# Performance work log

Hardware: AMD Instinct MI355X
Metric: run time of the kernel (lower is better)

The kernel has to match this reference:

```python
import jax, jax.numpy as jnp
import numpy as np

N_NODES = 100000
N_EDGES = 1600000
IN_DIM = 48
HID = 128
BN_EPS = 1e-5


def _batchnorm(h, gamma, beta):
    # BatchNorm1d in training mode: batch mean, biased variance
    mu = jnp.mean(h, axis=0)
    var = jnp.mean(jnp.square(h - mu), axis=0)
    return (h - mu) * jax.lax.rsqrt(var + BN_EPS) * gamma + beta


def setup_inputs() -> dict:
    key = jax.random.key(0)
    ks = jax.random.split(key, 8)
    x = jax.random.normal(ks[0], (N_NODES, IN_DIM), dtype=jnp.float32)
    edge_index = jax.random.randint(ks[1], (2, N_EDGES), 0, N_NODES, dtype=jnp.int64)
    s1 = 1.0 / np.sqrt(IN_DIM)
    s2 = 1.0 / np.sqrt(HID)
    return {
        "x": x,
        "edge_index": edge_index,
        "W1": jax.random.uniform(ks[2], (HID, IN_DIM), jnp.float32, -s1, s1),
        "b1": jnp.zeros((HID,), jnp.float32),
        "g1": jnp.ones((HID,), jnp.float32),
        "be1": jnp.zeros((HID,), jnp.float32),
        "Wl": jax.random.uniform(ks[3], (HID, HID), jnp.float32, -s2, s2),
        "bl": jnp.zeros((HID,), jnp.float32),
        "Wr": jax.random.uniform(ks[4], (HID, HID), jnp.float32, -s2, s2),
        "g2": jnp.ones((HID,), jnp.float32),
        "be2": jnp.zeros((HID,), jnp.float32),
    }


def reference(x, edge_index, W1, b1, g1, be1, Wl, bl, Wr, g2, be2):
    # input projection: Linear -> BatchNorm -> ReLU
    h = x @ W1.T + b1                               # [N, HID]
    feat = jax.nn.relu(_batchnorm(h, g1, be1))      # [N, HID]

    # SAGEConv (mean aggregation): messages flow src -> dst
    src, dst = edge_index[0], edge_index[1]
    summed = jax.ops.segment_sum(feat[src], dst, num_segments=N_NODES)  # [N, HID]
    cnt = jax.ops.segment_sum(jnp.ones((N_EDGES,), jnp.float32), dst, num_segments=N_NODES)
    agg = summed / jnp.maximum(cnt, 1.0)[:, None]
    sage = agg @ Wl.T + bl + feat @ Wr.T            # lin_l(mean) + lin_r(self)

    out_feat = _batchnorm(sage, g2, be2)
    return (feat, out_feat)
```

## Files before the change

### kernel.cpp

```cpp
#include <hip/hip_runtime.h>
#include <hip/hip_bf16.h>

#define NN 100000
#define NE 1600000
#define INDIM 48
#define HID 128
#define K2 256
#define KP 64
#define BN_EPS 1e-5f

#define NBUK 782
#define BCAP 2816
#define CHUNK 8192

#define MT ((NN + 63) / 64)
#define MT2 ((NN + 127) / 128)

typedef short s8v __attribute__((ext_vector_type(8)));
typedef float f4v __attribute__((ext_vector_type(4)));
typedef float f2v __attribute__((ext_vector_type(2)));

__device__ __forceinline__ unsigned short f2bf(float f) {
    __hip_bfloat16 b = __float2bfloat16(f);
    unsigned short u;
    __builtin_memcpy(&u, &b, 2);
    return u;
}
__device__ __forceinline__ float bflo(unsigned u) { return __uint_as_float(u << 16); }
__device__ __forceinline__ float bfhi(unsigned u) { return __uint_as_float(u & 0xffff0000u); }
__device__ __forceinline__ unsigned packbf(float lo, float hi) {
    return (unsigned)f2bf(lo) | ((unsigned)f2bf(hi) << 16);
}

__global__ __launch_bounds__(256) void k_xcast(const float* __restrict__ x,
                                               unsigned short* __restrict__ xbf,
                                               const float* __restrict__ Wl, const float* __restrict__ Wr,
                                               const float* __restrict__ W1,
                                               unsigned short* __restrict__ Wcat,
                                               unsigned short* __restrict__ W1b,
                                               int* __restrict__ bcur, float* __restrict__ stats) {
  int i = blockIdx.x * 256 + threadIdx.x;
  if (i < NN * 16) {
    int r = i >> 4, c4 = (i & 15) << 2;
    ushort4 o = {0, 0, 0, 0};
    if (c4 < INDIM) {
      float4 v = *(const float4*)(x + (size_t)r * INDIM + c4);
      o.x = f2bf(v.x);
      o.y = f2bf(v.y);
      o.z = f2bf(v.z);
      o.w = f2bf(v.w);
    }
    *(ushort4*)(xbf + (size_t)r * KP + c4) = o;
  }
  if (i < HID * K2) {
    int j = i >> 8, k = i & (K2 - 1);
    float v = (k < HID) ? Wl[j * HID + k] : Wr[j * HID + (k - HID)];
    Wcat[i] = f2bf(v);
  }
  int i2 = i - HID * K2;
  if (i2 >= 0 && i2 < HID * KP) {
    int j = i2 >> 6, k = i2 & (KP - 1);
    W1b[i2] = (k < INDIM) ? f2bf(W1[j * INDIM + k]) : (unsigned short)0;
  }
  int i3 = i2 - HID * KP;
  if (i3 >= 0 && i3 < NBUK) bcur[i3] = 0;
  int i4 = i3 - NBUK;
  if (i4 >= 0 && i4 < 4 * HID) stats[i4] = 0.f;
}

__global__ __launch_bounds__(256) void k_proj_gemm(
    const unsigned short* __restrict__ xbf, const unsigned short* __restrict__ W1b,
    const float* __restrict__ b1, unsigned short* __restrict__ Abuf,
    float* __restrict__ colSum, float* __restrict__ colSq) {
  __shared__ __align__(16) unsigned short Bsh[HID][KP + 8];
  __shared__ float redS[4][HID], redQ[4][HID];
  int tid = threadIdx.x;
  for (int i = tid; i < HID * (KP / 8); i += 256) {
    int j = i >> 3, kg = (i & 7) << 3;
    *(s8v*)&Bsh[j][kg] = *(const s8v*)(W1b + (size_t)j * KP + kg);
  }
  __syncthreads();
  int w = tid >> 6, l = tid & 63;
  int m16 = l & 15, q = l >> 4;
  float bcol[8];
#pragma unroll
  for (int nt = 0; nt < 8; ++nt) bcol[nt] = b1[nt * 16 + m16];
  float ssum[8], ssq[8];
#pragma unroll
  for (int nt = 0; nt < 8; ++nt) { ssum[nt] = 0.f; ssq[nt] = 0.f; }
  f4v zero4 = {0.f, 0.f, 0.f, 0.f};
  s8v zero8 = {0, 0, 0, 0, 0, 0, 0, 0};
  for (int tile = blockIdx.x; tile < MT; tile += gridDim.x) {
    int row = tile * 64 + w * 16 + m16;
    bool rv = row < NN;
    f4v acc[8];
#pragma unroll
    for (int nt = 0; nt < 8; ++nt) acc[nt] = zero4;
#pragma unroll
    for (int kt = 0; kt < 2; ++kt) {
      s8v a = zero8;
      if (rv) a = *(const s8v*)(xbf + (size_t)row * KP + kt * 32 + q * 8);
#pragma unroll
      for (int nt = 0; nt < 8; ++nt) {
        s8v b = *(const s8v*)(&Bsh[nt * 16 + m16][kt * 32 + q * 8]);
        acc[nt] = __builtin_amdgcn_mfma_f32_16x16x32_bf16(a, b, acc[nt], 0, 0, 0);
      }
    }
    int rbase = tile * 64 + w * 16 + q * 4;
#pragma unroll
    for (int nt = 0; nt < 8; ++nt) {
      int col = nt * 16 + m16;
#pragma unroll
      for (int r4 = 0; r4 < 4; ++r4) {
        int rr = rbase + r4;
        if (rr < NN) {
          float v = acc[nt][r4] + bcol[nt];
          Abuf[(size_t)rr * K2 + HID + col] = f2bf(v);
          ssum[nt] += v;
          ssq[nt] = fmaf(v, v, ssq[nt]);
        }
      }
    }
  }
#pragma unroll
  for (int nt = 0; nt < 8; ++nt) {
    float s = ssum[nt], qq = ssq[nt];
    s += __shfl_xor(s, 16);
    s += __shfl_xor(s, 32);
    qq += __shfl_xor(qq, 16);
    qq += __shfl_xor(qq, 32);
    if (q == 0) {
      redS[w][nt * 16 + m16] = s;
      redQ[w][nt * 16 + m16] = qq;
    }
  }
  __syncthreads();
  if (tid < HID) {
    float s = redS[0][tid] + redS[1][tid] + redS[2][tid] + redS[3][tid];
    float qq = redQ[0][tid] + redQ[1][tid] + redQ[2][tid] + redQ[3][tid];
    atomicAdd(&colSum[tid], s);
    atomicAdd(&colSq[tid], qq);
  }
}

__global__ void k_bn_final(const float* __restrict__ sum, const float* __restrict__ sq,
                           const float* __restrict__ gamma, const float* __restrict__ beta,
                           float* __restrict__ av, float* __restrict__ bv) {
  int c = threadIdx.x;
  float mu = sum[c] * (1.0f / NN);
  float var = fmaxf(sq[c] * (1.0f / NN) - mu * mu, 0.f);
  float a = gamma[c] * rsqrtf(var + BN_EPS);
  av[c] = a;
  bv[c] = beta[c] - mu * a;
}

__global__ __launch_bounds__(256) void k_apply(float* __restrict__ feat,
                                               const float* __restrict__ av,
                                               const float* __restrict__ bv,
                                               unsigned short* __restrict__ A,
                                               unsigned char* __restrict__ feat8) {
  int i = blockIdx.x * 256 + threadIdx.x;
  if (i >= NN * 16) return;
  int r = i >> 4, c8 = (i & 15) << 3;
  unsigned short* ap = A + (size_t)r * K2 + HID + c8;
  uint4 hv = *(const uint4*)ap;
  float4 a0 = *(const float4*)(av + c8);
  float4 a1 = *(const float4*)(av + c8 + 4);
  float4 b0 = *(const float4*)(bv + c8);
  float4 b1 = *(const float4*)(bv + c8 + 4);
  float f0 = fmaxf(fmaf(bflo(hv.x), a0.x, b0.x), 0.f);
  float f1 = fmaxf(fmaf(bfhi(hv.x), a0.y, b0.y), 0.f);
  float f2 = fmaxf(fmaf(bflo(hv.y), a0.z, b0.z), 0.f);
  float f3 = fmaxf(fmaf(bfhi(hv.y), a0.w, b0.w), 0.f);
  float f4 = fmaxf(fmaf(bflo(hv.z), a1.x, b1.x), 0.f);
  float f5 = fmaxf(fmaf(bfhi(hv.z), a1.y, b1.y), 0.f);
  float f6 = fmaxf(fmaf(bflo(hv.w), a1.z, b1.z), 0.f);
  float f7 = fmaxf(fmaf(bfhi(hv.w), a1.w, b1.w), 0.f);
  float4 o0 = {f0, f1, f2, f3}, o1 = {f4, f5, f6, f7};
  *(float4*)(feat + (size_t)r * HID + c8) = o0;
  *(float4*)(feat + (size_t)r * HID + c8 + 4) = o1;
  uint4 ob;
  ob.x = packbf(f0, f1);
  ob.y = packbf(f2, f3);
  ob.z = packbf(f4, f5);
  ob.w = packbf(f6, f7);
  *(uint4*)ap = ob;
  unsigned p0 = __builtin_amdgcn_cvt_pk_fp8_f32(f0, f1, 0u, false);
  p0 = __builtin_amdgcn_cvt_pk_fp8_f32(f2, f3, p0, true);
  unsigned p1 = __builtin_amdgcn_cvt_pk_fp8_f32(f4, f5, 0u, false);
  p1 = __builtin_amdgcn_cvt_pk_fp8_f32(f6, f7, p1, true);
  uint2 o8 = {p0, p1};
  *(uint2*)(feat8 + (size_t)r * HID + c8) = o8;
}

__global__ __launch_bounds__(512) void k_bucket(const int* __restrict__ ei,
                                                int* __restrict__ bcur,
                                                unsigned int* __restrict__ bbuf) {
  __shared__ int cnt[1024];
  __shared__ int sc[2][1024];
  __shared__ int ofs[1024];
  __shared__ int lcur[1024];
  __shared__ int gbase[1024];
  __shared__ unsigned int stag[CHUNK];
  __shared__ unsigned short sbkt[CHUNK];
  int tid = threadIdx.x;
  int base = blockIdx.x * CHUNK;
  int lim = min(CHUNK, NE - base);
  cnt[tid] = 0;
  cnt[tid + 512] = 0;
  __syncthreads();
#pragma unroll
  for (int i = 0; i < CHUNK / 512; ++i) {
    int e = i * 512 + tid;
    if (e < lim) {
      int d = ei[NE + base + e];
      d = min(max(d, 0), NN - 1);
      atomicAdd(&cnt[d >> 7], 1);
    }
  }
  __syncthreads();
  sc[0][tid] = cnt[tid];
  sc[0][tid + 512] = cnt[tid + 512];
  __syncthreads();
  int pp = 0;
  for (int d = 1; d < 1024; d <<= 1) {
    int a0 = sc[pp][tid];
    int a1 = sc[pp][tid + 512];
    if (tid >= d) a0 += sc[pp][tid - d];
    a1 += sc[pp][tid + 512 - d];
    sc[pp ^ 1][tid] = a0;
    sc[pp ^ 1][tid + 512] = a1;
    __syncthreads();
    pp ^= 1;
  }
  ofs[tid] = sc[pp][tid] - cnt[tid];
  ofs[tid + 512] = sc[pp][tid + 512] - cnt[tid + 512];
  lcur[tid] = ofs[tid];
  lcur[tid + 512] = ofs[tid + 512];
  if (tid < NBUK) gbase[tid] = atomicAdd(&bcur[tid], cnt[tid]);
  if (tid + 512 < NBUK) gbase[tid + 512] = atomicAdd(&bcur[tid + 512], cnt[tid + 512]);
  __syncthreads();
#pragma unroll
  for (int i = 0; i < CHUNK / 512; ++i) {
    int e = i * 512 + tid;
    if (e < lim) {
      int s = ei[base + e];
      int d = ei[NE + base + e];
      s = min(max(s, 0), NN - 1);
      d = min(max(d, 0), NN - 1);
      int b = d >> 7;
      int pos = atomicAdd(&lcur[b], 1);
      stag[pos] = (unsigned)s | ((unsigned)(d & 127) << 17);
      sbkt[pos] = (unsigned short)b;
    }
  }
  __syncthreads();
  for (int s = tid; s < lim; s += 512) {
    int b = sbkt[s];
    int off = gbase[b] + (s - ofs[b]);
    if (off < BCAP) bbuf[(size_t)b * BCAP + off] = stag[s];
  }
}

__global__ __launch_bounds__(512) void k_bucket_agg(const unsigned int* __restrict__ bbuf,
                                                    const int* __restrict__ bcnt,
                                                    const unsigned char* __restrict__ feat8,
                                                    unsigned short* __restrict__ Abuf) {
  __shared__ unsigned int lcsr[BCAP];
  __shared__ int cnt[128], ofs[128], cur[128];
  __shared__ int sc[2][128];
  int tid = threadIdx.x;
  int b = blockIdx.x;
  int m = min(bcnt[b], BCAP);
  int n0 = b << 7;
  int nb = min(128, NN - n0);
  if (tid < 128) cnt[tid] = 0;
  __syncthreads();
  const unsigned int* bp = bbuf + (size_t)b * BCAP;
  for (int s = tid; s < m; s += 512) {
    unsigned p = bp[s];
    atomicAdd(&cnt[(p >> 17) & 127], 1);
  }
  __syncthreads();
  if (tid < 128) sc[0][tid] = cnt[tid];
  __syncthreads();
  int pp = 0;
  for (int d = 1; d < 128; d <<= 1) {
    if (tid < 128) {
      int v = sc[pp][tid];
      if (tid >= d) v += sc[pp][tid - d];
      sc[pp ^ 1][tid] = v;
    }
    __syncthreads();
    pp ^= 1;
  }
  if (tid < 128) {
    int o = sc[pp][tid] - cnt[tid];
    ofs[tid] = o;
    cur[tid] = o;
  }
  __syncthreads();
  for (int s = tid; s < m; s += 512) {
    unsigned p = bp[s];
    int ld = (p >> 17) & 127;
    int pos = atomicAdd(&cur[ld], 1);
    lcsr[pos] = p & 0x1FFFF;
  }
  __syncthreads();
  int lane = tid & 31;
  int g = tid >> 5;
  int half = (lane >> 3) & 3;
  int l8 = lane & 7;
  for (int ln = g; ln < nb; ln += 16) {
    int deg = cnt[ln], beg = ofs[ln];
    float ac[16];
#pragma unroll
    for (int i = 0; i < 16; ++i) ac[i] = 0.f;
#pragma unroll 2
    for (int j = 0; j < deg; j += 4) {
      int idx = j + half;
      uint4 v = {0u, 0u, 0u, 0u};
      if (idx < deg) {
        int s = lcsr[beg + idx];
        v = *(const uint4*)(feat8 + (size_t)s * HID + l8 * 16);
      }
      f2v d;
      d = __builtin_amdgcn_cvt_pk_f32_fp8(v.x, false); ac[0] += d.x;  ac[1] += d.y;
      d = __builtin_amdgcn_cvt_pk_f32_fp8(v.x, true);  ac[2] += d.x;  ac[3] += d.y;
      d = __builtin_amdgcn_cvt_pk_f32_fp8(v.y, false); ac[4] += d.x;  ac[5] += d.y;
      d = __builtin_amdgcn_cvt_pk_f32_fp8(v.y, true);  ac[6] += d.x;  ac[7] += d.y;
      d = __builtin_amdgcn_cvt_pk_f32_fp8(v.z, false); ac[8] += d.x;  ac[9] += d.y;
      d = __builtin_amdgcn_cvt_pk_f32_fp8(v.z, true);  ac[10] += d.x; ac[11] += d.y;
      d = __builtin_amdgcn_cvt_pk_f32_fp8(v.w, false); ac[12] += d.x; ac[13] += d.y;
      d = __builtin_amdgcn_cvt_pk_f32_fp8(v.w, true);  ac[14] += d.x; ac[15] += d.y;
    }
#pragma unroll
    for (int i = 0; i < 16; ++i) {
      ac[i] += __shfl_xor(ac[i], 8);
      ac[i] += __shfl_xor(ac[i], 16);
    }
    if (half == 0) {
      float inv = 1.f / fmaxf((float)deg, 1.f);
      uint4 o0, o1;
      o0.x = packbf(ac[0] * inv, ac[1] * inv);
      o0.y = packbf(ac[2] * inv, ac[3] * inv);
      o0.z = packbf(ac[4] * inv, ac[5] * inv);
      o0.w = packbf(ac[6] * inv, ac[7] * inv);
      o1.x = packbf(ac[8] * inv, ac[9] * inv);
      o1.y = packbf(ac[10] * inv, ac[11] * inv);
      o1.z = packbf(ac[12] * inv, ac[13] * inv);
      o1.w = packbf(ac[14] * inv, ac[15] * inv);
      unsigned short* op = Abuf + (size_t)(n0 + ln) * K2 + l8 * 16;
      *(uint4*)op = o0;
      *(uint4*)(op + 8) = o1;
    }
  }
}

__global__ __launch_bounds__(512) void k_gemm(
    const unsigned short* __restrict__ A, const unsigned short* __restrict__ Wcat,
    const float* __restrict__ bl, unsigned short* __restrict__ sageb,
    float* __restrict__ colSum, float* __restrict__ colSq) {
  __shared__ __align__(16) unsigned short Bsh[HID][264];
  __shared__ float redS[8][HID], redQ[8][HID];
  int tid = threadIdx.x;
  for (int i = tid; i < HID * 32; i += 512) {
    int j = i >> 5;
    int kg = (i & 31) << 3;
    *(s8v*)&Bsh[j][kg] = *(const s8v*)(Wcat + (size_t)j * K2 + kg);
  }
  __syncthreads();
  int w = tid >> 6, l = tid & 63;
  int m16 = l & 15, q = l >> 4;
  int tile = blockIdx.x;
  int row = tile * 128 + w * 16 + m16;
  bool rv = row < NN;
  f4v zero4 = {0.f, 0.f, 0.f, 0.f};
  s8v zero8 = {0, 0, 0, 0, 0, 0, 0, 0};
  f4v acc[8];
#pragma unroll
  for (int nt = 0; nt < 8; ++nt) acc[nt] = zero4;
#pragma unroll
  for (int kt = 0; kt < 8; ++kt) {
    s8v a = zero8;
    if (rv) a = *(const s8v*)(A + (size_t)row * K2 + kt * 32 + q * 8);
#pragma unroll
    for (int nt = 0; nt < 8; ++nt) {
      s8v bfr = *(const s8v*)(&Bsh[nt * 16 + m16][kt * 32 + q * 8]);
      acc[nt] = __builtin_amdgcn_mfma_f32_16x16x32_bf16(a, bfr, acc[nt], 0, 0, 0);
    }
  }
  int rbase = tile * 128 + w * 16 + q * 4;
  float ssum[8], ssq[8];
#pragma unroll
  for (int nt = 0; nt < 8; ++nt) { ssum[nt] = 0.f; ssq[nt] = 0.f; }
#pragma unroll
  for (int nt = 0; nt < 8; ++nt) {
    int col = nt * 16 + m16;
    float bv = bl[col];
#pragma unroll
    for (int r4 = 0; r4 < 4; ++r4) {
      int rr = rbase + r4;
      if (rr < NN) {
        float v = acc[nt][r4] + bv;
        sageb[(size_t)rr * HID + col] = f2bf(v);
        ssum[nt] += v;
        ssq[nt] = fmaf(v, v, ssq[nt]);
      }
    }
  }
#pragma unroll
  for (int nt = 0; nt < 8; ++nt) {
    float s = ssum[nt], qq = ssq[nt];
    s += __shfl_xor(s, 16);
    s += __shfl_xor(s, 32);
    qq += __shfl_xor(qq, 16);
    qq += __shfl_xor(qq, 32);
    if (q == 0) {
      redS[w][nt * 16 + m16] = s;
      redQ[w][nt * 16 + m16] = qq;
    }
  }
  __syncthreads();
  if (tid < HID) {
    float s = 0.f, qq = 0.f;
#pragma unroll
    for (int ww = 0; ww < 8; ++ww) { s += redS[ww][tid]; qq += redQ[ww][tid]; }
    atomicAdd(&colSum[tid], s);
    atomicAdd(&colSq[tid], qq);
  }
}

__global__ __launch_bounds__(256) void k_bn_apply(const unsigned short* __restrict__ sageb,
                                                  float* __restrict__ out,
                                                  const float* __restrict__ av,
                                                  const float* __restrict__ bv) {
  int i = blockIdx.x * 256 + threadIdx.x;
  if (i >= NN * 16) return;
  int r = i >> 4, c8 = (i & 15) << 3;
  uint4 sv = *(const uint4*)(sageb + (size_t)r * HID + c8);
  float4 a0 = *(const float4*)(av + c8);
  float4 a1 = *(const float4*)(av + c8 + 4);
  float4 b0 = *(const float4*)(bv + c8);
  float4 b1 = *(const float4*)(bv + c8 + 4);
  float4 o0, o1;
  o0.x = fmaf(bflo(sv.x), a0.x, b0.x);
  o0.y = fmaf(bfhi(sv.x), a0.y, b0.y);
  o0.z = fmaf(bflo(sv.y), a0.z, b0.z);
  o0.w = fmaf(bfhi(sv.y), a0.w, b0.w);
  o1.x = fmaf(bflo(sv.z), a1.x, b1.x);
  o1.y = fmaf(bfhi(sv.z), a1.y, b1.y);
  o1.z = fmaf(bflo(sv.w), a1.z, b1.z);
  o1.w = fmaf(bfhi(sv.w), a1.w, b1.w);
  *(float4*)(out + (size_t)r * HID + c8) = o0;
  *(float4*)(out + (size_t)r * HID + c8 + 4) = o1;
}

extern "C" void kernel_launch(void* const* d_in, const int* in_sizes, int n_in,
                              void* d_out, int out_size, void* d_ws, size_t ws_size,
                              hipStream_t stream) {
  const float* x   = (const float*)d_in[0];
  const int*   ei  = (const int*)d_in[1];
  const float* W1  = (const float*)d_in[2];
  const float* b1  = (const float*)d_in[3];
  const float* g1  = (const float*)d_in[4];
  const float* be1 = (const float*)d_in[5];
  const float* Wl  = (const float*)d_in[6];
  const float* bl  = (const float*)d_in[7];
  const float* Wr  = (const float*)d_in[8];
  const float* g2  = (const float*)d_in[9];
  const float* be2 = (const float*)d_in[10];

  float* feat_out = (float*)d_out;
  float* out2     = (float*)d_out + (size_t)NN * HID;

  size_t off = 0;
  auto alloc = [&](size_t bytes) -> void* {
    void* p = (char*)d_ws + off;
    off += (bytes + 255) & ~(size_t)255;
    return p;
  };
  unsigned short* Abuf = (unsigned short*)alloc((size_t)NN * K2 * 2);
  unsigned char*  feat8 = (unsigned char*)alloc((size_t)NN * HID);
  unsigned short* sageb = (unsigned short*)alloc((size_t)NN * HID * 2);
  unsigned int*   bbuf = (unsigned int*)alloc((size_t)NBUK * BCAP * 4);
  int*            bcur = (int*)alloc((size_t)NBUK * 4);
  float*          stats = (float*)alloc(8 * HID * 4);
  float* colSum1 = stats;
  float* colSq1  = stats + HID;
  float* colSum2 = stats + 2 * HID;
  float* colSq2  = stats + 3 * HID;
  float* a1v     = stats + 4 * HID;
  float* b1v     = stats + 5 * HID;
  float* a2v     = stats + 6 * HID;
  float* b2v     = stats + 7 * HID;
  unsigned short* Wcat = (unsigned short*)alloc((size_t)HID * K2 * 2);
  unsigned short* W1b  = (unsigned short*)alloc((size_t)HID * KP * 2);
  unsigned short* xbf  = (unsigned short*)alloc((size_t)NN * KP * 2);

  k_xcast<<<(NN * 16 + 255) / 256, 256, 0, stream>>>(x, xbf, Wl, Wr, W1, Wcat, W1b, bcur, stats);
  k_bucket<<<(NE + CHUNK - 1) / CHUNK, 512, 0, stream>>>(ei, bcur, bbuf);
  k_proj_gemm<<<512, 256, 0, stream>>>(xbf, W1b, b1, Abuf, colSum1, colSq1);
  k_bn_final<<<1, HID, 0, stream>>>(colSum1, colSq1, g1, be1, a1v, b1v);
  k_apply<<<(NN * 16 + 255) / 256, 256, 0, stream>>>(feat_out, a1v, b1v, Abuf, feat8);
  k_bucket_agg<<<NBUK, 512, 0, stream>>>(bbuf, bcur, feat8, Abuf);
  k_gemm<<<MT2, 512, 0, stream>>>(Abuf, Wcat, bl, sageb, colSum2, colSq2);
  k_bn_final<<<1, HID, 0, stream>>>(colSum2, colSq2, g2, be2, a2v, b2v);
  k_bn_apply<<<(NN * 16 + 255) / 256, 256, 0, stream>>>(sageb, out2, a2v, b2v);
}
```

Measured before the change: 293.0 us.

## Fuse prep kernels, cast x inside projection GEMM, fold BN finalize into apply

Removes the standalone x-to-bf16 cast kernel: the projection GEMM now loads fp32 x directly and converts to bf16 in registers. The weight conversion moves into extra blocks of the bucketing kernel, and the counter/stat zeroing becomes a memset. Both single-block BN finalize launches are removed, and every apply block recomputes the per-column scale and shift into shared memory. This cuts kernel launches and an intermediate buffer write and read, in exchange for redundant per-block BN math and unaligned-width fp32 loads in the GEMM.

New measurement: 289.5 us. About the same (-1.2%).

```diff
diff --git a/kernel.cpp b/kernel.cpp
--- a/kernel.cpp
+++ b/kernel.cpp
@@ -12,6 +12,8 @@
 #define NBUK 782
 #define BCAP 2816
 #define CHUNK 8192
+#define NBB 196
+#define NPB 16
 
 #define MT ((NN + 63) / 64)
 #define MT2 ((NN + 127) / 128)
@@ -32,44 +34,95 @@
     return (unsigned)f2bf(lo) | ((unsigned)f2bf(hi) << 16);
 }
 
-__global__ __launch_bounds__(256) void k_xcast(const float* __restrict__ x,
-                                               unsigned short* __restrict__ xbf,
-                                               const float* __restrict__ Wl, const float* __restrict__ Wr,
-                                               const float* __restrict__ W1,
-                                               unsigned short* __restrict__ Wcat,
-                                               unsigned short* __restrict__ W1b,
-                                               int* __restrict__ bcur, float* __restrict__ stats) {
-  int i = blockIdx.x * 256 + threadIdx.x;
-  if (i < NN * 16) {
-    int r = i >> 4, c4 = (i & 15) << 2;
-    ushort4 o = {0, 0, 0, 0};
-    if (c4 < INDIM) {
-      float4 v = *(const float4*)(x + (size_t)r * INDIM + c4);
-      o.x = f2bf(v.x);
-      o.y = f2bf(v.y);
-      o.z = f2bf(v.z);
-      o.w = f2bf(v.w);
-    }
-    *(ushort4*)(xbf + (size_t)r * KP + c4) = o;
-  }
-  if (i < HID * K2) {
-    int j = i >> 8, k = i & (K2 - 1);
-    float v = (k < HID) ? Wl[j * HID + k] : Wr[j * HID + (k - HID)];
-    Wcat[i] = f2bf(v);
-  }
-  int i2 = i - HID * K2;
-  if (i2 >= 0 && i2 < HID * KP) {
-    int j = i2 >> 6, k = i2 & (KP - 1);
-    W1b[i2] = (k < INDIM) ? f2bf(W1[j * INDIM + k]) : (unsigned short)0;
-  }
-  int i3 = i2 - HID * KP;
-  if (i3 >= 0 && i3 < NBUK) bcur[i3] = 0;
-  int i4 = i3 - NBUK;
-  if (i4 >= 0 && i4 < 4 * HID) stats[i4] = 0.f;
+__global__ __launch_bounds__(512) void k_bucket_prep(const int* __restrict__ ei,
+                                                     int* __restrict__ bcur,
+                                                     unsigned int* __restrict__ bbuf,
+                                                     const float* __restrict__ Wl,
+                                                     const float* __restrict__ Wr,
+                                                     const float* __restrict__ W1,
+                                                     unsigned short* __restrict__ Wcat,
+                                                     unsigned short* __restrict__ W1b) {
+  int tid = threadIdx.x;
+  if (blockIdx.x >= NBB) {
+    int t0 = (blockIdx.x - NBB) * 512 + tid;
+    for (int i = t0; i < HID * K2; i += NPB * 512) {
+      int j = i >> 8, k = i & (K2 - 1);
+      float v = (k < HID) ? Wl[j * HID + k] : Wr[j * HID + (k - HID)];
+      Wcat[i] = f2bf(v);
+    }
+    for (int i = t0; i < HID * KP; i += NPB * 512) {
+      int j = i >> 6, k = i & (KP - 1);
+      W1b[i] = (k < INDIM) ? f2bf(W1[j * INDIM + k]) : (unsigned short)0;
+    }
+    return;
+  }
+  __shared__ int cnt[1024];
+  __shared__ int sc[2][1024];
+  __shared__ int ofs[1024];
+  __shared__ int lcur[1024];
+  __shared__ int gbase[1024];
+  __shared__ unsigned int stag[CHUNK];
+  __shared__ unsigned short sbkt[CHUNK];
+  int base = blockIdx.x * CHUNK;
+  int lim = min(CHUNK, NE - base);
+  cnt[tid] = 0;
+  cnt[tid + 512] = 0;
+  __syncthreads();
+#pragma unroll
+  for (int i = 0; i < CHUNK / 512; ++i) {
+    int e = i * 512 + tid;
+    if (e < lim) {
+      int d = ei[NE + base + e];
+      d = min(max(d, 0), NN - 1);
+      atomicAdd(&cnt[d >> 7], 1);
+    }
+  }
+  __syncthreads();
+  sc[0][tid] = cnt[tid];
+  sc[0][tid + 512] = cnt[tid + 512];
+  __syncthreads();
+  int pp = 0;
+  for (int d = 1; d < 1024; d <<= 1) {
+    int a0 = sc[pp][tid];
+    int a1 = sc[pp][tid + 512];
+    if (tid >= d) a0 += sc[pp][tid - d];
+    a1 += sc[pp][tid + 512 - d];
+    sc[pp ^ 1][tid] = a0;
+    sc[pp ^ 1][tid + 512] = a1;
+    __syncthreads();
+    pp ^= 1;
+  }
+  ofs[tid] = sc[pp][tid] - cnt[tid];
+  ofs[tid + 512] = sc[pp][tid + 512] - cnt[tid + 512];
+  lcur[tid] = ofs[tid];
+  lcur[tid + 512] = ofs[tid + 512];
+  if (tid < NBUK) gbase[tid] = atomicAdd(&bcur[tid], cnt[tid]);
+  if (tid + 512 < NBUK) gbase[tid + 512] = atomicAdd(&bcur[tid + 512], cnt[tid + 512]);
+  __syncthreads();
+#pragma unroll
+  for (int i = 0; i < CHUNK / 512; ++i) {
+    int e = i * 512 + tid;
+    if (e < lim) {
+      int s = ei[base + e];
+      int d = ei[NE + base + e];
+      s = min(max(s, 0), NN - 1);
+      d = min(max(d, 0), NN - 1);
+      int b = d >> 7;
+      int pos = atomicAdd(&lcur[b], 1);
+      stag[pos] = (unsigned)s | ((unsigned)(d & 127) << 17);
+      sbkt[pos] = (unsigned short)b;
+    }
+  }
+  __syncthreads();
+  for (int s = tid; s < lim; s += 512) {
+    int b = sbkt[s];
+    int off = gbase[b] + (s - ofs[b]);
+    if (off < BCAP) bbuf[(size_t)b * BCAP + off] = stag[s];
+  }
 }
 
 __global__ __launch_bounds__(256) void k_proj_gemm(
-    const unsigned short* __restrict__ xbf, const unsigned short* __restrict__ W1b,
+    const float* __restrict__ x, const unsigned short* __restrict__ W1b,
     const float* __restrict__ b1, unsigned short* __restrict__ Abuf,
     float* __restrict__ colSum, float* __restrict__ colSq) {
   __shared__ __align__(16) unsigned short Bsh[HID][KP + 8];
@@ -93,13 +146,22 @@
   for (int tile = blockIdx.x; tile < MT; tile += gridDim.x) {
     int row = tile * 64 + w * 16 + m16;
     bool rv = row < NN;
+    const float* xr = x + (size_t)row * INDIM;
     f4v acc[8];
 #pragma unroll
     for (int nt = 0; nt < 8; ++nt) acc[nt] = zero4;
 #pragma unroll
     for (int kt = 0; kt < 2; ++kt) {
+      int c0 = kt * 32 + q * 8;
       s8v a = zero8;
-      if (rv) a = *(const s8v*)(xbf + (size_t)row * KP + kt * 32 + q * 8);
+      if (rv && c0 < INDIM) {
+        float4 v0 = *(const float4*)(xr + c0);
+        float4 v1 = *(const float4*)(xr + c0 + 4);
+        a[0] = (short)f2bf(v0.x); a[1] = (short)f2bf(v0.y);
+        a[2] = (short)f2bf(v0.z); a[3] = (short)f2bf(v0.w);
+        a[4] = (short)f2bf(v1.x); a[5] = (short)f2bf(v1.y);
+        a[6] = (short)f2bf(v1.z); a[7] = (short)f2bf(v1.w);
+      }
 #pragma unroll
       for (int nt = 0; nt < 8; ++nt) {
         s8v b = *(const s8v*)(&Bsh[nt * 16 + m16][kt * 32 + q * 8]);
@@ -143,31 +205,32 @@
   }
 }
 
-__global__ void k_bn_final(const float* __restrict__ sum, const float* __restrict__ sq,
-                           const float* __restrict__ gamma, const float* __restrict__ beta,
-                           float* __restrict__ av, float* __restrict__ bv) {
-  int c = threadIdx.x;
-  float mu = sum[c] * (1.0f / NN);
-  float var = fmaxf(sq[c] * (1.0f / NN) - mu * mu, 0.f);
-  float a = gamma[c] * rsqrtf(var + BN_EPS);
-  av[c] = a;
-  bv[c] = beta[c] - mu * a;
-}
-
 __global__ __launch_bounds__(256) void k_apply(float* __restrict__ feat,
-                                               const float* __restrict__ av,
-                                               const float* __restrict__ bv,
+                                               const float* __restrict__ colSum,
+                                               const float* __restrict__ colSq,
+                                               const float* __restrict__ g1,
+                                               const float* __restrict__ be1,
                                                unsigned short* __restrict__ A,
                                                unsigned char* __restrict__ feat8) {
-  int i = blockIdx.x * 256 + threadIdx.x;
+  __shared__ __align__(16) float sa[HID], sb[HID];
+  int tid = threadIdx.x;
+  if (tid < HID) {
+    float mu = colSum[tid] * (1.0f / NN);
+    float var = fmaxf(colSq[tid] * (1.0f / NN) - mu * mu, 0.f);
+    float a = g1[tid] * rsqrtf(var + BN_EPS);
+    sa[tid] = a;
+    sb[tid] = be1[tid] - mu * a;
+  }
+  __syncthreads();
+  int i = blockIdx.x * 256 + tid;
   if (i >= NN * 16) return;
   int r = i >> 4, c8 = (i & 15) << 3;
   unsigned short* ap = A + (size_t)r * K2 + HID + c8;
   uint4 hv = *(const uint4*)ap;
-  float4 a0 = *(const float4*)(av + c8);
-  float4 a1 = *(const float4*)(av + c8 + 4);
-  float4 b0 = *(const float4*)(bv + c8);
-  float4 b1 = *(const float4*)(bv + c8 + 4);
+  float4 a0 = *(const float4*)(sa + c8);
+  float4 a1 = *(const float4*)(sa + c8 + 4);
+  float4 b0 = *(const float4*)(sb + c8);
+  float4 b1 = *(const float4*)(sb + c8 + 4);
   float f0 = fmaxf(fmaf(bflo(hv.x), a0.x, b0.x), 0.f);
   float f1 = fmaxf(fmaf(bfhi(hv.x), a0.y, b0.y), 0.f);
   float f2 = fmaxf(fmaf(bflo(hv.y), a0.z, b0.z), 0.f);
@@ -193,75 +256,6 @@
   *(uint2*)(feat8 + (size_t)r * HID + c8) = o8;
 }
 
-__global__ __launch_bounds__(512) void k_bucket(const int* __restrict__ ei,
-                                                int* __restrict__ bcur,
-                                                unsigned int* __restrict__ bbuf) {
-  __shared__ int cnt[1024];
-  __shared__ int sc[2][1024];
-  __shared__ int ofs[1024];
-  __shared__ int lcur[1024];
-  __shared__ int gbase[1024];
-  __shared__ unsigned int stag[CHUNK];
-  __shared__ unsigned short sbkt[CHUNK];
-  int tid = threadIdx.x;
-  int base = blockIdx.x * CHUNK;
-  int lim = min(CHUNK, NE - base);
-  cnt[tid] = 0;
-  cnt[tid + 512] = 0;
-  __syncthreads();
-#pragma unroll
-  for (int i = 0; i < CHUNK / 512; ++i) {
-    int e = i * 512 + tid;
-    if (e < lim) {
-      int d = ei[NE + base + e];
-      d = min(max(d, 0), NN - 1);
-      atomicAdd(&cnt[d >> 7], 1);
-    }
-  }
-  __syncthreads();
-  sc[0][tid] = cnt[tid];
-  sc[0][tid + 512] = cnt[tid + 512];
-  __syncthreads();
-  int pp = 0;
-  for (int d = 1; d < 1024; d <<= 1) {
-    int a0 = sc[pp][tid];
-    int a1 = sc[pp][tid + 512];
-    if (tid >= d) a0 += sc[pp][tid - d];
-    a1 += sc[pp][tid + 512 - d];
-    sc[pp ^ 1][tid] = a0;
-    sc[pp ^ 1][tid + 512] = a1;
-    __syncthreads();
-    pp ^= 1;
-  }
-  ofs[tid] = sc[pp][tid] - cnt[tid];
-  ofs[tid + 512] = sc[pp][tid + 512] - cnt[tid + 512];
-  lcur[tid] = ofs[tid];
-  lcur[tid + 512] = ofs[tid + 512];
-  if (tid < NBUK) gbase[tid] = atomicAdd(&bcur[tid], cnt[tid]);
-  if (tid + 512 < NBUK) gbase[tid + 512] = atomicAdd(&bcur[tid + 512], cnt[tid + 512]);
-  __syncthreads();
-#pragma unroll
-  for (int i = 0; i < CHUNK / 512; ++i) {
-    int e = i * 512 + tid;
-    if (e < lim) {
-      int s = ei[base + e];
-      int d = ei[NE + base + e];
-      s = min(max(s, 0), NN - 1);
-      d = min(max(d, 0), NN - 1);
-      int b = d >> 7;
-      int pos = atomicAdd(&lcur[b], 1);
-      stag[pos] = (unsigned)s | ((unsigned)(d & 127) << 17);
-      sbkt[pos] = (unsigned short)b;
-    }
-  }
-  __syncthreads();
-  for (int s = tid; s < lim; s += 512) {
-    int b = sbkt[s];
-    int off = gbase[b] + (s - ofs[b]);
-    if (off < BCAP) bbuf[(size_t)b * BCAP + off] = stag[s];
-  }
-}
-
 __global__ __launch_bounds__(512) void k_bucket_agg(const unsigned int* __restrict__ bbuf,
                                                     const int* __restrict__ bcnt,
                                                     const unsigned char* __restrict__ feat8,
@@ -433,16 +427,28 @@
 
 __global__ __launch_bounds__(256) void k_bn_apply(const unsigned short* __restrict__ sageb,
                                                   float* __restrict__ out,
-                                                  const float* __restrict__ av,
-                                                  const float* __restrict__ bv) {
-  int i = blockIdx.x * 256 + threadIdx.x;
+                                                  const float* __restrict__ colSum,
+                                                  const float* __restrict__ colSq,
+                                                  const float* __restrict__ g2,
+                                                  const float* __restrict__ be2) {
+  __shared__ __align__(16) float sa[HID], sb[HID];
+  int tid = threadIdx.x;
+  if (tid < HID) {
+    float mu = colSum[tid] * (1.0f / NN);
+    float var = fmaxf(colSq[tid] * (1.0f / NN) - mu * mu, 0.f);
+    float a = g2[tid] * rsqrtf(var + BN_EPS);
+    sa[tid] = a;
+    sb[tid] = be2[tid] - mu * a;
+  }
+  __syncthreads();
+  int i = blockIdx.x * 256 + tid;
   if (i >= NN * 16) return;
   int r = i >> 4, c8 = (i & 15) << 3;
   uint4 sv = *(const uint4*)(sageb + (size_t)r * HID + c8);
-  float4 a0 = *(const float4*)(av + c8);
-  float4 a1 = *(const float4*)(av + c8 + 4);
-  float4 b0 = *(const float4*)(bv + c8);
-  float4 b1 = *(const float4*)(bv + c8 + 4);
+  float4 a0 = *(const float4*)(sa + c8);
+  float4 a1 = *(const float4*)(sa + c8 + 4);
+  float4 b0 = *(const float4*)(sb + c8);
+  float4 b1 = *(const float4*)(sb + c8 + 4);
   float4 o0, o1;
   o0.x = fmaf(bflo(sv.x), a0.x, b0.x);
   o0.y = fmaf(bfhi(sv.x), a0.y, b0.y);
@@ -480,31 +486,24 @@
     off += (bytes + 255) & ~(size_t)255;
     return p;
   };
-  unsigned short* Abuf = (unsigned short*)alloc((size_t)NN * K2 * 2);
+  float*          stats = (float*)alloc(4 * HID * 4);
+  int*            bcur  = (int*)alloc((size_t)NBUK * 4);
+  unsigned short* Abuf  = (unsigned short*)alloc((size_t)NN * K2 * 2);
   unsigned char*  feat8 = (unsigned char*)alloc((size_t)NN * HID);
   unsigned short* sageb = (unsigned short*)alloc((size_t)NN * HID * 2);
-  unsigned int*   bbuf = (unsigned int*)alloc((size_t)NBUK * BCAP * 4);
-  int*            bcur = (int*)alloc((size_t)NBUK * 4);
-  float*          stats = (float*)alloc(8 * HID * 4);
+  unsigned int*   bbuf  = (unsigned int*)alloc((size_t)NBUK * BCAP * 4);
+  unsigned short* Wcat  = (unsigned short*)alloc((size_t)HID * K2 * 2);
+  unsigned short* W1b   = (unsigned short*)alloc((size_t)HID * KP * 2);
   float* colSum1 = stats;
   float* colSq1  = stats + HID;
   float* colSum2 = stats + 2 * HID;
   float* colSq2  = stats + 3 * HID;
-  float* a1v     = stats + 4 * HID;
-  float* b1v     = stats + 5 * HID;
-  float* a2v     = stats + 6 * HID;
-  float* b2v     = stats + 7 * HID;
-  unsigned short* Wcat = (unsigned short*)alloc((size_t)HID * K2 * 2);
-  unsigned short* W1b  = (unsigned short*)alloc((size_t)HID * KP * 2);
-  unsigned short* xbf  = (unsigned short*)alloc((size_t)NN * KP * 2);
-
-  k_xcast<<<(NN * 16 + 255) / 256, 256, 0, stream>>>(x, xbf, Wl, Wr, W1, Wcat, W1b, bcur, stats);
-  k_bucket<<<(NE + CHUNK - 1) / CHUNK, 512, 0, stream>>>(ei, bcur, bbuf);
-  k_proj_gemm<<<512, 256, 0, stream>>>(xbf, W1b, b1, Abuf, colSum1, colSq1);
-  k_bn_final<<<1, HID, 0, stream>>>(colSum1, colSq1, g1, be1, a1v, b1v);
-  k_apply<<<(NN * 16 + 255) / 256, 256, 0, stream>>>(feat_out, a1v, b1v, Abuf, feat8);
+
+  hipMemsetAsync(stats, 0, 4 * HID * 4 + (size_t)NBUK * 4, stream);
+  k_bucket_prep<<<NBB + NPB, 512, 0, stream>>>(ei, bcur, bbuf, Wl, Wr, W1, Wcat, W1b);
+  k_proj_gemm<<<512, 256, 0, stream>>>(x, W1b, b1, Abuf, colSum1, colSq1);
+  k_apply<<<(NN * 16 + 255) / 256, 256, 0, stream>>>(feat_out, colSum1, colSq1, g1, be1, Abuf, feat8);
   k_bucket_agg<<<NBUK, 512, 0, stream>>>(bbuf, bcur, feat8, Abuf);
   k_gemm<<<MT2, 512, 0, stream>>>(Abuf, Wcat, bl, sageb, colSum2, colSq2);
-  k_bn_final<<<1, HID, 0, stream>>>(colSum2, colSq2, g2, be2, a2v, b2v);
-  k_bn_apply<<<(NN * 16 + 255) / 256, 256, 0, stream>>>(sageb, out2, a2v, b2v);
-}
+  k_bn_apply<<<(NN * 16 + 255) / 256, 256, 0, stream>>>(sageb, out2, colSum2, colSq2, g2, be2);
+}
```
